# Optimization experiments

Measured on AMD Instinct MI355X. Metric: run time of the kernel, lower is better.

The kernel has to match this reference:

```python
import jax, jax.numpy as jnp
import numpy as np

N = 10000        # nodes
E = 160000       # edges (before self-loops)
NFEAT = 256
NHID = 128
H = 4            # heads
NCLASS = 40
NLAYERS = 2
DT = 1.0
ALPHA = 1.0
GAMMA = 1.0
NEG_SLOPE = 0.2  # GATConv leaky_relu slope


def setup_inputs() -> dict:
    key = jax.random.key(0)
    ks = jax.random.split(key, 12)

    def glorot(k, shape):
        fan_in, fan_out = shape[-1], shape[0]
        lim = (6.0 / (fan_in + fan_out)) ** 0.5
        return jax.random.uniform(k, shape, jnp.float32, -lim, lim)

    return {
        "x": jax.random.normal(ks[0], (N, NFEAT), jnp.float32),
        "edge_index": jax.random.randint(ks[1], (2, E), 0, N, jnp.int64),
        "enc_w": glorot(ks[2], (NHID, NFEAT)),
        "enc_b": jnp.zeros((NHID,), jnp.float32),
        "res_w": glorot(ks[3], (H * NHID, NHID)),
        "res_b": jnp.zeros((H * NHID,), jnp.float32),
        "gat_w": glorot(ks[4], (H * NHID, NHID)),
        "att_src": glorot(ks[5], (H, NHID)) * 0.1,
        "att_dst": glorot(ks[6], (H, NHID)) * 0.1,
        "gat_b": jnp.zeros((H * NHID,), jnp.float32),
        "dec_w": glorot(ks[7], (NCLASS, NHID)),
        "dec_b": jnp.zeros((NCLASS,), jnp.float32),
    }


def _gat_conv(x, src, dst, gat_w, att_src, att_dst, gat_b):
    # x: [N, NHID] -> per-head features [N, H, C]
    xh = (x @ gat_w.T).reshape(N, H, NHID)
    a_src = jnp.sum(xh * att_src[None], axis=-1)  # [N, H]
    a_dst = jnp.sum(xh * att_dst[None], axis=-1)  # [N, H]
    e = jax.nn.leaky_relu(a_src[src] + a_dst[dst], NEG_SLOPE)  # [E', H]
    # segment softmax over incoming edges of each destination node
    m = jax.ops.segment_max(e, dst, num_segments=N)            # [N, H]
    e = jnp.exp(e - m[dst])
    s = jax.ops.segment_sum(e, dst, num_segments=N)            # [N, H]
    alpha = e / s[dst]                                          # [E', H]
    msg = xh[src] * alpha[:, :, None]                           # [E', H, C]
    out = jax.ops.segment_sum(msg, dst, num_segments=N)         # [N, H, C]
    return out.reshape(N, H * NHID) + gat_b


def reference(x, edge_index, enc_w, enc_b, res_w, res_b, gat_w,
              att_src, att_dst, gat_b, dec_w, dec_b):
    # add self-loops (GATConv default)
    loop = jnp.arange(N, dtype=edge_index.dtype)
    src = jnp.concatenate([edge_index[0], loop])
    dst = jnp.concatenate([edge_index[1], loop])

    Y = jax.nn.relu(x @ enc_w.T + enc_b)  # [N, NHID]
    X = Y
    for _ in range(NLAYERS):
        conv = _gat_conv(X, src, dst, gat_w, att_src, att_dst, gat_b)  # [N, H*NHID]
        res = X @ res_w.T + res_b                                       # [N, H*NHID]
        # faithful to .view(n_nodes, -1, nheads).mean(-1): [N, NHID, H] -> mean over heads axis
        z = jax.nn.elu(conv + res).reshape(N, NHID, H).mean(axis=-1)    # [N, NHID]
        Y = Y + DT * (z - ALPHA * Y - GAMMA * X)
        X = X + DT * Y
    return X @ dec_w.T + dec_b  # [N, NCLASS]
```

## Files before the change

kernel.cpp:

```cpp
#include <hip/hip_runtime.h>
#include <math.h>

#define NN 10000
#define EE 160000
#define EP 170000
#define NFEAT 256
#define NHID 128
#define NH 4
#define HF 512
#define NCLASS 40
#define FCOLS 1088

typedef __attribute__((ext_vector_type(8))) short bf8;
typedef __attribute__((ext_vector_type(8))) unsigned short u16x8;
typedef __attribute__((ext_vector_type(4))) float f4;

__device__ __forceinline__ float leaky02(float x) { return x >= 0.0f ? x : 0.2f * x; }

__device__ __forceinline__ unsigned short f2bf(float f) {
    unsigned u = __builtin_bit_cast(unsigned, f);
    unsigned r = (u + 0x7FFF + ((u >> 16) & 1)) >> 16;
    return (unsigned short)r;
}
__device__ __forceinline__ float bf2f(unsigned short h) {
    return __builtin_bit_cast(float, (unsigned)h << 16);
}

__device__ __forceinline__ int swz(int row, int c) {
    return ((((c >> 3) ^ (row & 7)) << 3) | (c & 7));
}

__device__ __forceinline__ void gl_lds16(const unsigned short* g, unsigned short* l)
{
    __builtin_amdgcn_global_load_lds(
        (const __attribute__((address_space(1))) unsigned int*)g,
        (__attribute__((address_space(3))) unsigned int*)l, 16, 0, 0);
}

#define C_X   2560000
#define C_EW  (C_X + 32768)
#define C_FW  (C_EW + 131072)
#define C_DW  (C_FW + 5120)
#define CVT_B  1333
#define ATTW_B (CVT_B + 8)
#define TOT_B  (ATTW_B + 166)

__global__ __launch_bounds__(256)
void fused0_k(const float* __restrict__ x, const float* __restrict__ enc_w,
              const float* __restrict__ gat_w, const float* __restrict__ res_w,
              const float* __restrict__ dec_w, const float* __restrict__ att_src,
              const float* __restrict__ att_dst, const float* __restrict__ res_b,
              const float* __restrict__ gat_b, const int* __restrict__ ei,
              unsigned short* __restrict__ xhi, unsigned short* __restrict__ xlo,
              unsigned short* __restrict__ ewhi, unsigned short* __restrict__ ewlo,
              unsigned short* __restrict__ fwhi, unsigned short* __restrict__ fwlo,
              unsigned short* __restrict__ dwhi, unsigned short* __restrict__ dwlo,
              float* __restrict__ biasRG, int* __restrict__ cnt)
{
    int bId = blockIdx.x;
    int t = threadIdx.x;
    if (bId < CVT_B) {
        int iu = bId * 256 + t;
        int i = iu * 8;
        if (i >= C_DW) return;
        const float* src = nullptr; unsigned short *ph, *pl; int j, row, c, Kd;
        if (i < C_X)       { j = i;        src = x;     ph = xhi;  pl = xlo;
                             row = j >> 8; c = j & 255; Kd = 256; }
        else if (i < C_EW) { j = i - C_X;  src = enc_w; ph = ewhi; pl = ewlo;
                             row = j >> 8; c = j & 255; Kd = 256; }
        else if (i < C_FW) { j = i - C_EW; ph = fwhi;   pl = fwlo;
                             row = j >> 7; c = j & 127; Kd = 128; }
        else               { j = i - C_FW; src = dec_w; ph = dwhi; pl = dwlo;
                             row = j >> 7; c = j & 127; Kd = 128; }
        float4 v0, v1;
        if (src) { v0 = *(const float4*)(src + j); v1 = *(const float4*)(src + j + 4); }
        else {
            const float* s2 = (j < 65536) ? (gat_w + j) : (res_w + j - 65536);
            v0 = *(const float4*)s2; v1 = *(const float4*)(s2 + 4);
        }
        float vv[8] = {v0.x, v0.y, v0.z, v0.w, v1.x, v1.y, v1.z, v1.w};
        unsigned short hs[8], ls[8];
#pragma unroll
        for (int k = 0; k < 8; ++k) {
            hs[k] = f2bf(vv[k]);
            ls[k] = f2bf(vv[k] - bf2f(hs[k]));
        }
        int outp = row * Kd + swz(row, c);
        *(u16x8*)(ph + outp) = *(u16x8*)hs;
        *(u16x8*)(pl + outp) = *(u16x8*)ls;
    } else if (bId < ATTW_B) {
        __shared__ float sm[256];
        int b = bId - CVT_B;
        int is_dst = b >> 2, h = b & 3;
        const float* att = is_dst ? att_dst : att_src;
        int k = t & 127, half = t >> 7;
        float s = 0.0f;
#pragma unroll 4
        for (int c = half * 64; c < half * 64 + 64; ++c)
            s = fmaf(gat_w[(size_t)(h * 128 + c) * 128 + k], att[h * 128 + c], s);
        sm[t] = s;
        __syncthreads();
        if (t < 128) {
            float v = sm[t] + sm[t + 128];
            int R = 1024 + is_dst * 4 + h;
            size_t o = (size_t)R * 128 + swz(R, k);
            unsigned short hi = f2bf(v);
            fwhi[o] = hi;
            fwlo[o] = f2bf(v - bf2f(hi));
        }
        for (int i = b * 896 + t; i < (b + 1) * 896; i += 256) {
            fwhi[1032 * 128 + i] = 0;
            fwlo[1032 * 128 + i] = 0;
        }
        if (b < 2) {
            int c = b * 256 + t;
            biasRG[c] = res_b[c] + gat_b[c];
        }
    } else {
        for (int e = (bId - ATTW_B) * 256 + t; e < EP; e += (TOT_B - ATTW_B) * 256) {
            int d = (e < EE) ? ei[EE + e] : (e - EE);
            atomicAdd(&cnt[d], 1);
        }
    }
}

template<int MODE, int KTILES, int MERGE>
__global__ __launch_bounds__(256)
void gemm3_k(const unsigned short* __restrict__ Ahi, const unsigned short* __restrict__ Alo,
             const unsigned short* __restrict__ Bhi, const unsigned short* __restrict__ Blo,
             const float* __restrict__ bias,
             float* __restrict__ outF, unsigned short* __restrict__ outH,
             unsigned short* __restrict__ outL,
             float* __restrict__ a_src, float* __restrict__ a_dst, int M,
             const int* __restrict__ ei, const int* __restrict__ cnt,
             int* __restrict__ row_ptr, int* __restrict__ cursor, int* __restrict__ csr)
{
    constexpr int K = KTILES * 128;
    __shared__ __align__(16) unsigned short smem[4 * 64 * 128];
    const int tid = threadIdx.x;

    if (MERGE && blockIdx.y == gridDim.y - 1) {
        if (MERGE == 1) {
            if (blockIdx.x != 0) return;
            int* smi = (int*)smem;
            int i0 = tid * 40, i1 = min(i0 + 40, NN);
            int part = 0;
            for (int i = i0; i < i1; ++i) part += cnt[i];
            smi[tid] = part;
            __syncthreads();
            for (int off = 1; off < 256; off <<= 1) {
                int v = (tid >= off) ? smi[tid - off] : 0;
                __syncthreads();
                smi[tid] += v;
                __syncthreads();
            }
            int run = smi[tid] - part;
            for (int i = i0; i < i1; ++i) { row_ptr[i] = run; run += cnt[i]; }
            if (tid == 255) row_ptr[NN] = run;
        } else {
            int stride = gridDim.x * 256;
            for (int e = blockIdx.x * 256 + tid; e < EP; e += stride) {
                int s, d;
                if (e < EE) { s = ei[e]; d = ei[EE + e]; } else { s = e - EE; d = s; }
                int pos = row_ptr[d] + atomicAdd(&cursor[d], 1);
                csr[pos] = s;
            }
        }
        return;
    }

    unsigned short* sAh = smem;
    unsigned short* sAl = smem + 8192;
    unsigned short* sBh = smem + 16384;
    unsigned short* sBl = smem + 24576;

    const int lane = tid & 63, wv = tid >> 6;
    const int wr = (wv >> 1) * 32, wc = (wv & 1) * 32;
    const int bm = blockIdx.x * 64, bn = blockIdx.y * 64;
    const int r16 = lane & 15, q4 = lane >> 4;

    f4 acc[2][2];
#pragma unroll
    for (int i = 0; i < 2; ++i)
#pragma unroll
        for (int j = 0; j < 2; ++j) acc[i][j] = (f4){0.f, 0.f, 0.f, 0.f};

    const int ra0 = wr + r16;
    const int rb0 = wc + r16;

    for (int kt = 0; kt < KTILES; ++kt) {
        if (kt) __syncthreads();
#pragma unroll
        for (int j = 0; j < 4; ++j) {
            int i = tid + j * 256;
            int row = i >> 4, u = i & 15;
            int arow = min(bm + row, M - 1);
            int brow = bn + row;
            size_t ga = (size_t)arow * K + kt * 128 + u * 8;
            size_t gb = (size_t)brow * K + kt * 128 + u * 8;
            int lb = (wv * 64 + j * 256) * 8;
            gl_lds16(Ahi + ga, sAh + lb);
            gl_lds16(Alo + ga, sAl + lb);
            gl_lds16(Bhi + gb, sBh + lb);
            gl_lds16(Blo + gb, sBl + lb);
        }
        __syncthreads();

#pragma unroll
        for (int ks = 0; ks < 4; ++ks) {
            int u = ks * 4 + q4;
            int oa0 = ra0 * 128 + ((u ^ (ra0 & 7)) * 8);
            int ob0 = rb0 * 128 + ((u ^ (rb0 & 7)) * 8);
            int oa1 = oa0 + 16 * 128;
            int ob1 = ob0 + 16 * 128;
            bf8 A0h = *(const bf8*)(sAh + oa0);
            bf8 A1h = *(const bf8*)(sAh + oa1);
            bf8 A0l = *(const bf8*)(sAl + oa0);
            bf8 A1l = *(const bf8*)(sAl + oa1);
            bf8 B0h = *(const bf8*)(sBh + ob0);
            bf8 B1h = *(const bf8*)(sBh + ob1);
            bf8 B0l = *(const bf8*)(sBl + ob0);
            bf8 B1l = *(const bf8*)(sBl + ob1);

            acc[0][0] = __builtin_amdgcn_mfma_f32_16x16x32_bf16(A0h, B0h, acc[0][0], 0, 0, 0);
            acc[0][1] = __builtin_amdgcn_mfma_f32_16x16x32_bf16(A0h, B1h, acc[0][1], 0, 0, 0);
            acc[1][0] = __builtin_amdgcn_mfma_f32_16x16x32_bf16(A1h, B0h, acc[1][0], 0, 0, 0);
            acc[1][1] = __builtin_amdgcn_mfma_f32_16x16x32_bf16(A1h, B1h, acc[1][1], 0, 0, 0);
            acc[0][0] = __builtin_amdgcn_mfma_f32_16x16x32_bf16(A0h, B0l, acc[0][0], 0, 0, 0);
            acc[0][1] = __builtin_amdgcn_mfma_f32_16x16x32_bf16(A0h, B1l, acc[0][1], 0, 0, 0);
            acc[1][0] = __builtin_amdgcn_mfma_f32_16x16x32_bf16(A1h, B0l, acc[1][0], 0, 0, 0);
            acc[1][1] = __builtin_amdgcn_mfma_f32_16x16x32_bf16(A1h, B1l, acc[1][1], 0, 0, 0);
            acc[0][0] = __builtin_amdgcn_mfma_f32_16x16x32_bf16(A0l, B0h, acc[0][0], 0, 0, 0);
            acc[0][1] = __builtin_amdgcn_mfma_f32_16x16x32_bf16(A0l, B1h, acc[0][1], 0, 0, 0);
            acc[1][0] = __builtin_amdgcn_mfma_f32_16x16x32_bf16(A1l, B0h, acc[1][0], 0, 0, 0);
            acc[1][1] = __builtin_amdgcn_mfma_f32_16x16x32_bf16(A1l, B1h, acc[1][1], 0, 0, 0);
        }
    }

    const int rbase = q4 * 4;

    if (MODE == 0 || (MODE == 2 && bn >= 1024)) {
#pragma unroll
        for (int i = 0; i < 2; ++i)
#pragma unroll
            for (int j = 0; j < 2; ++j)
#pragma unroll
                for (int r = 0; r < 4; ++r) {
                    int row = bm + wr + i * 16 + rbase + r;
                    int col = bn + wc + j * 16 + r16;
                    if (row >= M) continue;
                    float v = acc[i][j][r];
                    if (MODE == 0) {
                        if (col < NCLASS)
                            outF[(size_t)row * NCLASS + col] = v + bias[col];
                    } else {
                        if (col < 1032) {
                            int h = col - 1024;
                            if (h < 4) a_src[row * 4 + h] = v;
                            else       a_dst[row * 4 + h - 4] = v;
                        }
                    }
                }
        return;
    }

    __syncthreads();
    float* sC = (float*)smem;
#pragma unroll
    for (int i = 0; i < 2; ++i)
#pragma unroll
        for (int j = 0; j < 2; ++j)
#pragma unroll
            for (int r = 0; r < 4; ++r)
                sC[(wr + i * 16 + rbase + r) * 65 + (wc + j * 16 + r16)] = acc[i][j][r];
    __syncthreads();

    int row = tid >> 2, seg = tid & 3, c0 = seg * 16;
    int grow = bm + row;
    if (grow >= M) return;
    float v[16];
#pragma unroll
    for (int k = 0; k < 16; ++k) v[k] = sC[row * 65 + c0 + k];

    if (MODE == 1) {
        unsigned short hs[16], ls[16];
#pragma unroll
        for (int k = 0; k < 16; ++k) {
            float u = fmaxf(v[k] + bias[bn + c0 + k], 0.0f);
            hs[k] = f2bf(u);
            ls[k] = f2bf(u - bf2f(hs[k]));
        }
#pragma unroll
        for (int uu = 0; uu < 2; ++uu) {
            int ug = (bn + c0) / 8 + uu;
            int pu = ug ^ (grow & 7);
            *(u16x8*)(outH + (size_t)grow * 128 + pu * 8) = *(u16x8*)(hs + uu * 8);
            *(u16x8*)(outL + (size_t)grow * 128 + pu * 8) = *(u16x8*)(ls + uu * 8);
        }
    } else {
        if (bn < 512) {
            unsigned short hs[16];
#pragma unroll
            for (int k = 0; k < 16; ++k) hs[k] = f2bf(v[k]);
            *(u16x8*)(outH + (size_t)grow * 512 + bn + c0)     = *(u16x8*)hs;
            *(u16x8*)(outH + (size_t)grow * 512 + bn + c0 + 8) = *(u16x8*)(hs + 8);
        } else {
            unsigned short hs[16];
#pragma unroll
            for (int k = 0; k < 16; ++k) hs[k] = f2bf(v[k] + bias[bn - 512 + c0 + k]);
            *(u16x8*)(outL + (size_t)grow * 512 + (bn - 512) + c0)     = *(u16x8*)hs;
            *(u16x8*)(outL + (size_t)grow * 512 + (bn - 512) + c0 + 8) = *(u16x8*)(hs + 8);
        }
    }
}

__global__ __launch_bounds__(256)
void agg_k(const int* __restrict__ row_ptr, const int* __restrict__ csr,
           const float* __restrict__ a_src, const float* __restrict__ a_dst,
           const unsigned short* __restrict__ xh_b, const unsigned short* __restrict__ resb,
           unsigned short* __restrict__ Xhi, unsigned short* __restrict__ Xlo)
{
    __shared__ float sAcc[2][64][8];
    __shared__ float sSum[2][64];
    int wv = threadIdx.x >> 6, lane = threadIdx.x & 63;
    int pair = wv >> 1, half = wv & 1;
    int d = blockIdx.x * 2 + pair;
    int beg = row_ptr[d], end = row_ptr[d + 1];
    int len = end - beg;
    int h0 = (len + 1) >> 1;
    int eb = half ? (beg + h0) : beg;
    int en = half ? end : (beg + h0);
    int hl = lane >> 4;
    int cb = lane * 8;
    float ad = a_dst[d * 4 + hl];
    u16x8 rv = *(const u16x8*)(resb + (size_t)d * HF + cb);

    float acc[8];
#pragma unroll
    for (int k = 0; k < 8; ++k) acc[k] = 0.0f;
    float ssum = 0.0f;

    int e = eb;
    for (; e + 8 <= en; e += 8) {
        int sv[8]; float w[8]; u16x8 v[8];
#pragma unroll
        for (int q = 0; q < 8; ++q) sv[q] = csr[e + q];
#pragma unroll
        for (int q = 0; q < 8; ++q) v[q] = *(const u16x8*)(xh_b + (size_t)sv[q] * HF + cb);
#pragma unroll
        for (int q = 0; q < 8; ++q) {
            w[q] = __expf(leaky02(a_src[sv[q] * 4 + hl] + ad));
            ssum += w[q];
        }
#pragma unroll
        for (int q = 0; q < 8; ++q)
#pragma unroll
            for (int k = 0; k < 8; ++k) acc[k] = fmaf(w[q], bf2f(v[q][k]), acc[k]);
    }
    for (; e + 4 <= en; e += 4) {
        int sv[4]; float w[4]; u16x8 v[4];
#pragma unroll
        for (int q = 0; q < 4; ++q) sv[q] = csr[e + q];
#pragma unroll
        for (int q = 0; q < 4; ++q) v[q] = *(const u16x8*)(xh_b + (size_t)sv[q] * HF + cb);
#pragma unroll
        for (int q = 0; q < 4; ++q) {
            w[q] = __expf(leaky02(a_src[sv[q] * 4 + hl] + ad));
            ssum += w[q];
        }
#pragma unroll
        for (int q = 0; q < 4; ++q)
#pragma unroll
            for (int k = 0; k < 8; ++k) acc[k] = fmaf(w[q], bf2f(v[q][k]), acc[k]);
    }
    for (; e < en; ++e) {
        int s = csr[e];
        float w = __expf(leaky02(a_src[s * 4 + hl] + ad));
        ssum += w;
        u16x8 v = *(const u16x8*)(xh_b + (size_t)s * HF + cb);
#pragma unroll
        for (int k = 0; k < 8; ++k) acc[k] = fmaf(w, bf2f(v[k]), acc[k]);
    }

    if (half) {
        *(float4*)&sAcc[pair][lane][0] = make_float4(acc[0], acc[1], acc[2], acc[3]);
        *(float4*)&sAcc[pair][lane][4] = make_float4(acc[4], acc[5], acc[6], acc[7]);
        sSum[pair][lane] = ssum;
    }
    __syncthreads();
    if (half) return;
#pragma unroll
    for (int k = 0; k < 8; ++k) acc[k] += sAcc[pair][lane][k];
    ssum += sSum[pair][lane];

    float inv = 1.0f / ssum;
    float u[8];
#pragma unroll
    for (int k = 0; k < 8; ++k) {
        float v = fmaf(acc[k], inv, bf2f(rv[k]));
        u[k] = (v > 0.0f) ? v : expm1f(v);
    }
    float z0 = (u[0] + u[1] + u[2] + u[3]) * 0.25f;
    float z1 = (u[4] + u[5] + u[6] + u[7]) * 0.25f;
    unsigned short h0b = f2bf(z0), h1b = f2bf(z1);
    unsigned short l0b = f2bf(z0 - bf2f(h0b)), l1b = f2bf(z1 - bf2f(h1b));
    int pos = swz(d, lane * 2);
    size_t idx = (size_t)d * NHID + pos;
    *(unsigned*)(Xhi + idx) = ((unsigned)h1b << 16) | h0b;
    *(unsigned*)(Xlo + idx) = ((unsigned)l1b << 16) | l0b;
}

extern "C" void kernel_launch(void* const* d_in, const int* in_sizes, int n_in,
                              void* d_out, int out_size, void* d_ws, size_t ws_size,
                              hipStream_t stream)
{
    const float* x       = (const float*)d_in[0];
    const int*   ei      = (const int*)d_in[1];
    const float* enc_w   = (const float*)d_in[2];
    const float* enc_b   = (const float*)d_in[3];
    const float* res_w   = (const float*)d_in[4];
    const float* res_b   = (const float*)d_in[5];
    const float* gat_w   = (const float*)d_in[6];
    const float* att_src = (const float*)d_in[7];
    const float* att_dst = (const float*)d_in[8];
    const float* gat_b   = (const float*)d_in[9];
    const float* dec_w   = (const float*)d_in[10];
    const float* dec_b   = (const float*)d_in[11];
    float* out = (float*)d_out;

    char* p = (char*)d_ws;
    auto alloc = [&](size_t bytes) -> void* {
        void* r = (void*)p;
        p += (bytes + 255) & ~(size_t)255;
        return r;
    };
    float* a_src  = (float*)alloc(40000 * 4);
    float* a_dst  = (float*)alloc(40000 * 4);
    float* biasRG = (float*)alloc(512 * 4);
    unsigned short* xh_b = (unsigned short*)alloc(5120000 * 2);
    unsigned short* resb = (unsigned short*)alloc(5120000 * 2);
    unsigned short* Xhi  = (unsigned short*)alloc(1280000 * 2);
    unsigned short* Xlo  = (unsigned short*)alloc(1280000 * 2);
    unsigned short* xhi  = (unsigned short*)alloc(2560000 * 2);
    unsigned short* xlo  = (unsigned short*)alloc(2560000 * 2);
    unsigned short* ewhi = (unsigned short*)alloc(32768 * 2);
    unsigned short* ewlo = (unsigned short*)alloc(32768 * 2);
    unsigned short* fwhi = (unsigned short*)alloc(FCOLS * 128 * 2);
    unsigned short* fwlo = (unsigned short*)alloc(FCOLS * 128 * 2);
    int* row_ptr = (int*)alloc(10004 * 4);
    int* csr     = (int*)alloc(170000 * 4);
    char* zbase = p;
    unsigned short* dwhi = (unsigned short*)alloc(8192 * 2);
    unsigned short* dwlo = (unsigned short*)alloc(8192 * 2);
    int* cnt    = (int*)alloc(10000 * 4);
    int* cursor = (int*)alloc(10000 * 4);
    size_t zbytes = (size_t)(p - zbase);

    hipMemsetAsync(zbase, 0, zbytes, stream);

    fused0_k<<<TOT_B, 256, 0, stream>>>(
        x, enc_w, gat_w, res_w, dec_w, att_src, att_dst, res_b, gat_b, ei,
        xhi, xlo, ewhi, ewlo, fwhi, fwlo, dwhi, dwlo, biasRG, cnt);

    gemm3_k<1, 2, 1><<<dim3(157, 3), 256, 0, stream>>>(
        xhi, xlo, ewhi, ewlo, enc_b, nullptr, Xhi, Xlo, nullptr, nullptr, NN,
        nullptr, cnt, row_ptr, nullptr, nullptr);

    gemm3_k<2, 1, 2><<<dim3(157, 18), 256, 0, stream>>>(
        Xhi, Xlo, fwhi, fwlo, biasRG, nullptr, xh_b, resb, a_src, a_dst, NN,
        ei, nullptr, row_ptr, cursor, csr);
    agg_k<<<5000, 256, 0, stream>>>(row_ptr, csr, a_src, a_dst, xh_b, resb, Xhi, Xlo);

    gemm3_k<2, 1, 0><<<dim3(157, 17), 256, 0, stream>>>(
        Xhi, Xlo, fwhi, fwlo, biasRG, nullptr, xh_b, resb, a_src, a_dst, NN,
        nullptr, nullptr, nullptr, nullptr, nullptr);
    agg_k<<<5000, 256, 0, stream>>>(row_ptr, csr, a_src, a_dst, xh_b, resb, Xhi, Xlo);

    gemm3_k<0, 1, 0><<<dim3(157, 1), 256, 0, stream>>>(
        Xhi, Xlo, dwhi, dwlo, dec_b, out, nullptr, nullptr, nullptr, nullptr, NN,
        nullptr, nullptr, nullptr, nullptr, nullptr);
}
```

Measured before the change: 225.2 us.

## Reuse A tile across two N-tiles in GEMM; split aggregation across four waves

Each GEMM block now loads its A tile once per k-step and computes two 64-column output tiles against it, which halves redundant A traffic and the number of blocks in the grid. The aggregation kernel moves from two nodes per block (two waves each) to one node per block with four waves, each taking a quarter of the incoming edges, and their partial sums are combined through LDS. The residual load is deferred until after the reduction. This adds more syncs per block, more accumulator registers, and fewer GEMM blocks, which can lower occupancy and leave the GPU less well filled.

```diff
diff --git a/kernel.cpp b/kernel.cpp
--- a/kernel.cpp
+++ b/kernel.cpp
@@ -136,6 +136,7 @@
              int* __restrict__ row_ptr, int* __restrict__ cursor, int* __restrict__ csr)
 {
     constexpr int K = KTILES * 128;
+    constexpr int NBT = (MODE == 1) ? 2 : (MODE == 2) ? 17 : 1;
     __shared__ __align__(16) unsigned short smem[4 * 64 * 128];
     const int tid = threadIdx.x;
 
@@ -176,140 +177,155 @@
 
     const int lane = tid & 63, wv = tid >> 6;
     const int wr = (wv >> 1) * 32, wc = (wv & 1) * 32;
-    const int bm = blockIdx.x * 64, bn = blockIdx.y * 64;
+    const int bm = blockIdx.x * 64;
+    const int t0 = blockIdx.y * 2;
+    const int nS = (NBT - t0 < 2) ? (NBT - t0) : 2;
     const int r16 = lane & 15, q4 = lane >> 4;
 
-    f4 acc[2][2];
-#pragma unroll
-    for (int i = 0; i < 2; ++i)
-#pragma unroll
-        for (int j = 0; j < 2; ++j) acc[i][j] = (f4){0.f, 0.f, 0.f, 0.f};
+    f4 acc[2][2][2];
+#pragma unroll
+    for (int s = 0; s < 2; ++s)
+#pragma unroll
+        for (int i = 0; i < 2; ++i)
+#pragma unroll
+            for (int j = 0; j < 2; ++j) acc[s][i][j] = (f4){0.f, 0.f, 0.f, 0.f};
 
     const int ra0 = wr + r16;
     const int rb0 = wc + r16;
 
     for (int kt = 0; kt < KTILES; ++kt) {
-        if (kt) __syncthreads();
 #pragma unroll
         for (int j = 0; j < 4; ++j) {
             int i = tid + j * 256;
             int row = i >> 4, u = i & 15;
             int arow = min(bm + row, M - 1);
-            int brow = bn + row;
             size_t ga = (size_t)arow * K + kt * 128 + u * 8;
-            size_t gb = (size_t)brow * K + kt * 128 + u * 8;
             int lb = (wv * 64 + j * 256) * 8;
             gl_lds16(Ahi + ga, sAh + lb);
             gl_lds16(Alo + ga, sAl + lb);
-            gl_lds16(Bhi + gb, sBh + lb);
-            gl_lds16(Blo + gb, sBl + lb);
-        }
-        __syncthreads();
-
-#pragma unroll
-        for (int ks = 0; ks < 4; ++ks) {
-            int u = ks * 4 + q4;
-            int oa0 = ra0 * 128 + ((u ^ (ra0 & 7)) * 8);
-            int ob0 = rb0 * 128 + ((u ^ (rb0 & 7)) * 8);
-            int oa1 = oa0 + 16 * 128;
-            int ob1 = ob0 + 16 * 128;
-            bf8 A0h = *(const bf8*)(sAh + oa0);
-            bf8 A1h = *(const bf8*)(sAh + oa1);
-            bf8 A0l = *(const bf8*)(sAl + oa0);
-            bf8 A1l = *(const bf8*)(sAl + oa1);
-            bf8 B0h = *(const bf8*)(sBh + ob0);
-            bf8 B1h = *(const bf8*)(sBh + ob1);
-            bf8 B0l = *(const bf8*)(sBl + ob0);
-            bf8 B1l = *(const bf8*)(sBl + ob1);
-
-            acc[0][0] = __builtin_amdgcn_mfma_f32_16x16x32_bf16(A0h, B0h, acc[0][0], 0, 0, 0);
-            acc[0][1] = __builtin_amdgcn_mfma_f32_16x16x32_bf16(A0h, B1h, acc[0][1], 0, 0, 0);
-            acc[1][0] = __builtin_amdgcn_mfma_f32_16x16x32_bf16(A1h, B0h, acc[1][0], 0, 0, 0);
-            acc[1][1] = __builtin_amdgcn_mfma_f32_16x16x32_bf16(A1h, B1h, acc[1][1], 0, 0, 0);
-            acc[0][0] = __builtin_amdgcn_mfma_f32_16x16x32_bf16(A0h, B0l, acc[0][0], 0, 0, 0);
-            acc[0][1] = __builtin_amdgcn_mfma_f32_16x16x32_bf16(A0h, B1l, acc[0][1], 0, 0, 0);
-            acc[1][0] = __builtin_amdgcn_mfma_f32_16x16x32_bf16(A1h, B0l, acc[1][0], 0, 0, 0);
-            acc[1][1] = __builtin_amdgcn_mfma_f32_16x16x32_bf16(A1h, B1l, acc[1][1], 0, 0, 0);
-            acc[0][0] = __builtin_amdgcn_mfma_f32_16x16x32_bf16(A0l, B0h, acc[0][0], 0, 0, 0);
-            acc[0][1] = __builtin_amdgcn_mfma_f32_16x16x32_bf16(A0l, B1h, acc[0][1], 0, 0, 0);
-            acc[1][0] = __builtin_amdgcn_mfma_f32_16x16x32_bf16(A1l, B0h, acc[1][0], 0, 0, 0);
-            acc[1][1] = __builtin_amdgcn_mfma_f32_16x16x32_bf16(A1l, B1h, acc[1][1], 0, 0, 0);
+        }
+        for (int s = 0; s < nS; ++s) {
+            int bn = (t0 + s) * 64;
+#pragma unroll
+            for (int j = 0; j < 4; ++j) {
+                int i = tid + j * 256;
+                int row = i >> 4, u = i & 15;
+                size_t gb = (size_t)(bn + row) * K + kt * 128 + u * 8;
+                int lb = (wv * 64 + j * 256) * 8;
+                gl_lds16(Bhi + gb, sBh + lb);
+                gl_lds16(Blo + gb, sBl + lb);
+            }
+            __syncthreads();
+#pragma unroll
+            for (int ks = 0; ks < 4; ++ks) {
+                int u = ks * 4 + q4;
+                int oa0 = ra0 * 128 + ((u ^ (ra0 & 7)) * 8);
+                int ob0 = rb0 * 128 + ((u ^ (rb0 & 7)) * 8);
+                int oa1 = oa0 + 16 * 128;
+                int ob1 = ob0 + 16 * 128;
+                bf8 A0h = *(const bf8*)(sAh + oa0);
+                bf8 A1h = *(const bf8*)(sAh + oa1);
+                bf8 A0l = *(const bf8*)(sAl + oa0);
+                bf8 A1l = *(const bf8*)(sAl + oa1);
+                bf8 B0h = *(const bf8*)(sBh + ob0);
+                bf8 B1h = *(const bf8*)(sBh + ob1);
+                bf8 B0l = *(const bf8*)(sBl + ob0);
+                bf8 B1l = *(const bf8*)(sBl + ob1);
+
+                acc[s][0][0] = __builtin_amdgcn_mfma_f32_16x16x32_bf16(A0h, B0h, acc[s][0][0], 0, 0, 0);
+                acc[s][0][1] = __builtin_amdgcn_mfma_f32_16x16x32_bf16(A0h, B1h, acc[s][0][1], 0, 0, 0);
+                acc[s][1][0] = __builtin_amdgcn_mfma_f32_16x16x32_bf16(A1h, B0h, acc[s][1][0], 0, 0, 0);
+                acc[s][1][1] = __builtin_amdgcn_mfma_f32_16x16x32_bf16(A1h, B1h, acc[s][1][1], 0, 0, 0);
+                acc[s][0][0] = __builtin_amdgcn_mfma_f32_16x16x32_bf16(A0h, B0l, acc[s][0][0], 0, 0, 0);
+                acc[s][0][1] = __builtin_amdgcn_mfma_f32_16x16x32_bf16(A0h, B1l, acc[s][0][1], 0, 0, 0);
+                acc[s][1][0] = __builtin_amdgcn_mfma_f32_16x16x32_bf16(A1h, B0l, acc[s][1][0], 0, 0, 0);
+                acc[s][1][1] = __builtin_amdgcn_mfma_f32_16x16x32_bf16(A1h, B1l, acc[s][1][1], 0, 0, 0);
+                acc[s][0][0] = __builtin_amdgcn_mfma_f32_16x16x32_bf16(A0l, B0h, acc[s][0][0], 0, 0, 0);
+                acc[s][0][1] = __builtin_amdgcn_mfma_f32_16x16x32_bf16(A0l, B1h, acc[s][0][1], 0, 0, 0);
+                acc[s][1][0] = __builtin_amdgcn_mfma_f32_16x16x32_bf16(A1l, B0h, acc[s][1][0], 0, 0, 0);
+                acc[s][1][1] = __builtin_amdgcn_mfma_f32_16x16x32_bf16(A1l, B1h, acc[s][1][1], 0, 0, 0);
+            }
+            __syncthreads();
         }
     }
 
     const int rbase = q4 * 4;
 
-    if (MODE == 0 || (MODE == 2 && bn >= 1024)) {
-#pragma unroll
-        for (int i = 0; i < 2; ++i)
-#pragma unroll
-            for (int j = 0; j < 2; ++j)
-#pragma unroll
-                for (int r = 0; r < 4; ++r) {
-                    int row = bm + wr + i * 16 + rbase + r;
-                    int col = bn + wc + j * 16 + r16;
-                    if (row >= M) continue;
-                    float v = acc[i][j][r];
-                    if (MODE == 0) {
-                        if (col < NCLASS)
-                            outF[(size_t)row * NCLASS + col] = v + bias[col];
-                    } else {
-                        if (col < 1032) {
-                            int h = col - 1024;
-                            if (h < 4) a_src[row * 4 + h] = v;
-                            else       a_dst[row * 4 + h - 4] = v;
+    for (int s = 0; s < nS; ++s) {
+        int bn = (t0 + s) * 64;
+        if (MODE == 0 || (MODE == 2 && bn >= 1024)) {
+#pragma unroll
+            for (int i = 0; i < 2; ++i)
+#pragma unroll
+                for (int j = 0; j < 2; ++j)
+#pragma unroll
+                    for (int r = 0; r < 4; ++r) {
+                        int row = bm + wr + i * 16 + rbase + r;
+                        int col = bn + wc + j * 16 + r16;
+                        if (row >= M) continue;
+                        float v = acc[s][i][j][r];
+                        if (MODE == 0) {
+                            if (col < NCLASS)
+                                outF[(size_t)row * NCLASS + col] = v + bias[col];
+                        } else {
+                            if (col < 1032) {
+                                int h = col - 1024;
+                                if (h < 4) a_src[row * 4 + h] = v;
+                                else       a_dst[row * 4 + h - 4] = v;
+                            }
                         }
                     }
+            continue;
+        }
+
+        __syncthreads();
+        float* sC = (float*)smem;
+#pragma unroll
+        for (int i = 0; i < 2; ++i)
+#pragma unroll
+            for (int j = 0; j < 2; ++j)
+#pragma unroll
+                for (int r = 0; r < 4; ++r)
+                    sC[(wr + i * 16 + rbase + r) * 65 + (wc + j * 16 + r16)] = acc[s][i][j][r];
+        __syncthreads();
+
+        int row = tid >> 2, seg = tid & 3, c0 = seg * 16;
+        int grow = bm + row;
+        if (grow < M) {
+            float v[16];
+#pragma unroll
+            for (int k = 0; k < 16; ++k) v[k] = sC[row * 65 + c0 + k];
+
+            if (MODE == 1) {
+                unsigned short hs[16], ls[16];
+#pragma unroll
+                for (int k = 0; k < 16; ++k) {
+                    float u = fmaxf(v[k] + bias[bn + c0 + k], 0.0f);
+                    hs[k] = f2bf(u);
+                    ls[k] = f2bf(u - bf2f(hs[k]));
                 }
-        return;
-    }
-
-    __syncthreads();
-    float* sC = (float*)smem;
-#pragma unroll
-    for (int i = 0; i < 2; ++i)
-#pragma unroll
-        for (int j = 0; j < 2; ++j)
-#pragma unroll
-            for (int r = 0; r < 4; ++r)
-                sC[(wr + i * 16 + rbase + r) * 65 + (wc + j * 16 + r16)] = acc[i][j][r];
-    __syncthreads();
-
-    int row = tid >> 2, seg = tid & 3, c0 = seg * 16;
-    int grow = bm + row;
-    if (grow >= M) return;
-    float v[16];
-#pragma unroll
-    for (int k = 0; k < 16; ++k) v[k] = sC[row * 65 + c0 + k];
-
-    if (MODE == 1) {
-        unsigned short hs[16], ls[16];
-#pragma unroll
-        for (int k = 0; k < 16; ++k) {
-            float u = fmaxf(v[k] + bias[bn + c0 + k], 0.0f);
-            hs[k] = f2bf(u);
-            ls[k] = f2bf(u - bf2f(hs[k]));
-        }
-#pragma unroll
-        for (int uu = 0; uu < 2; ++uu) {
-            int ug = (bn + c0) / 8 + uu;
-            int pu = ug ^ (grow & 7);
-            *(u16x8*)(outH + (size_t)grow * 128 + pu * 8) = *(u16x8*)(hs + uu * 8);
-            *(u16x8*)(outL + (size_t)grow * 128 + pu * 8) = *(u16x8*)(ls + uu * 8);
-        }
-    } else {
-        if (bn < 512) {
-            unsigned short hs[16];
-#pragma unroll
-            for (int k = 0; k < 16; ++k) hs[k] = f2bf(v[k]);
-            *(u16x8*)(outH + (size_t)grow * 512 + bn + c0)     = *(u16x8*)hs;
-            *(u16x8*)(outH + (size_t)grow * 512 + bn + c0 + 8) = *(u16x8*)(hs + 8);
-        } else {
-            unsigned short hs[16];
-#pragma unroll
-            for (int k = 0; k < 16; ++k) hs[k] = f2bf(v[k] + bias[bn - 512 + c0 + k]);
-            *(u16x8*)(outL + (size_t)grow * 512 + (bn - 512) + c0)     = *(u16x8*)hs;
-            *(u16x8*)(outL + (size_t)grow * 512 + (bn - 512) + c0 + 8) = *(u16x8*)(hs + 8);
+#pragma unroll
+                for (int uu = 0; uu < 2; ++uu) {
+                    int ug = (bn + c0) / 8 + uu;
+                    int pu = ug ^ (grow & 7);
+                    *(u16x8*)(outH + (size_t)grow * 128 + pu * 8) = *(u16x8*)(hs + uu * 8);
+                    *(u16x8*)(outL + (size_t)grow * 128 + pu * 8) = *(u16x8*)(ls + uu * 8);
+                }
+            } else {
+                if (bn < 512) {
+                    unsigned short hs[16];
+#pragma unroll
+                    for (int k = 0; k < 16; ++k) hs[k] = f2bf(v[k]);
+                    *(u16x8*)(outH + (size_t)grow * 512 + bn + c0)     = *(u16x8*)hs;
+                    *(u16x8*)(outH + (size_t)grow * 512 + bn + c0 + 8) = *(u16x8*)(hs + 8);
+                } else {
+                    unsigned short hs[16];
+#pragma unroll
+                    for (int k = 0; k < 16; ++k) hs[k] = f2bf(v[k] + bias[bn - 512 + c0 + k]);
+                    *(u16x8*)(outL + (size_t)grow * 512 + (bn - 512) + c0)     = *(u16x8*)hs;
+                    *(u16x8*)(outL + (size_t)grow * 512 + (bn - 512) + c0 + 8) = *(u16x8*)(hs + 8);
+                }
+            }
         }
     }
 }
@@ -320,20 +336,17 @@
            const unsigned short* __restrict__ xh_b, const unsigned short* __restrict__ resb,
            unsigned short* __restrict__ Xhi, unsigned short* __restrict__ Xlo)
 {
-    __shared__ float sAcc[2][64][8];
-    __shared__ float sSum[2][64];
+    __shared__ float sAcc[3][64][8];
+    __shared__ float sSum[3][64];
     int wv = threadIdx.x >> 6, lane = threadIdx.x & 63;
-    int pair = wv >> 1, half = wv & 1;
-    int d = blockIdx.x * 2 + pair;
+    int d = blockIdx.x;
     int beg = row_ptr[d], end = row_ptr[d + 1];
     int len = end - beg;
-    int h0 = (len + 1) >> 1;
-    int eb = half ? (beg + h0) : beg;
-    int en = half ? end : (beg + h0);
+    int eb = beg + (len * wv) / 4;
+    int en = beg + (len * (wv + 1)) / 4;
     int hl = lane >> 4;
     int cb = lane * 8;
     float ad = a_dst[d * 4 + hl];
-    u16x8 rv = *(const u16x8*)(resb + (size_t)d * HF + cb);
 
     float acc[8];
 #pragma unroll
@@ -382,16 +395,21 @@
         for (int k = 0; k < 8; ++k) acc[k] = fmaf(w, bf2f(v[k]), acc[k]);
     }
 
-    if (half) {
-        *(float4*)&sAcc[pair][lane][0] = make_float4(acc[0], acc[1], acc[2], acc[3]);
-        *(float4*)&sAcc[pair][lane][4] = make_float4(acc[4], acc[5], acc[6], acc[7]);
-        sSum[pair][lane] = ssum;
+    if (wv) {
+        *(float4*)&sAcc[wv - 1][lane][0] = make_float4(acc[0], acc[1], acc[2], acc[3]);
+        *(float4*)&sAcc[wv - 1][lane][4] = make_float4(acc[4], acc[5], acc[6], acc[7]);
+        sSum[wv - 1][lane] = ssum;
     }
     __syncthreads();
-    if (half) return;
-#pragma unroll
-    for (int k = 0; k < 8; ++k) acc[k] += sAcc[pair][lane][k];
-    ssum += sSum[pair][lane];
+    if (wv) return;
+
+    u16x8 rv = *(const u16x8*)(resb + (size_t)d * HF + cb);
+#pragma unroll
+    for (int p = 0; p < 3; ++p) {
+#pragma unroll
+        for (int k = 0; k < 8; ++k) acc[k] += sAcc[p][lane][k];
+        ssum += sSum[p][lane];
+    }
 
     float inv = 1.0f / ssum;
     float u[8];
@@ -462,19 +480,19 @@
         x, enc_w, gat_w, res_w, dec_w, att_src, att_dst, res_b, gat_b, ei,
         xhi, xlo, ewhi, ewlo, fwhi, fwlo, dwhi, dwlo, biasRG, cnt);
 
-    gemm3_k<1, 2, 1><<<dim3(157, 3), 256, 0, stream>>>(
+    gemm3_k<1, 2, 1><<<dim3(157, 2), 256, 0, stream>>>(
         xhi, xlo, ewhi, ewlo, enc_b, nullptr, Xhi, Xlo, nullptr, nullptr, NN,
         nullptr, cnt, row_ptr, nullptr, nullptr);
 
-    gemm3_k<2, 1, 2><<<dim3(157, 18), 256, 0, stream>>>(
+    gemm3_k<2, 1, 2><<<dim3(157, 10), 256, 0, stream>>>(
         Xhi, Xlo, fwhi, fwlo, biasRG, nullptr, xh_b, resb, a_src, a_dst, NN,
         ei, nullptr, row_ptr, cursor, csr);
-    agg_k<<<5000, 256, 0, stream>>>(row_ptr, csr, a_src, a_dst, xh_b, resb, Xhi, Xlo);
-
-    gemm3_k<2, 1, 0><<<dim3(157, 17), 256, 0, stream>>>(
+    agg_k<<<NN, 256, 0, stream>>>(row_ptr, csr, a_src, a_dst, xh_b, resb, Xhi, Xlo);
+
+    gemm3_k<2, 1, 0><<<dim3(157, 9), 256, 0, stream>>>(
         Xhi, Xlo, fwhi, fwlo, biasRG, nullptr, xh_b, resb, a_src, a_dst, NN,
         nullptr, nullptr, nullptr, nullptr, nullptr);
-    agg_k<<<5000, 256, 0, stream>>>(row_ptr, csr, a_src, a_dst, xh_b, resb, Xhi, Xlo);
+    agg_k<<<NN, 256, 0, stream>>>(row_ptr, csr, a_src, a_dst, xh_b, resb, Xhi, Xlo);
 
     gemm3_k<0, 1, 0><<<dim3(157, 1), 256, 0, stream>>>(
         Xhi, Xlo, dwhi, dwlo, dec_b, out, nullptr, nullptr, nullptr, nullptr, NN,
```

Result: slower. 240.0 us (+6.6%).
